# Performance work log

Hardware: AMD Instinct MI355X
Metric: run time of the kernel (lower is better)

## Reference

```python
import jax, jax.numpy as jnp
import numpy as np

B, S, D, H = 2, 2048, 1024, 16
DK = D // H

def setup_inputs() -> dict:
    key = jax.random.key(0)
    ks = jax.random.split(key, 11)
    scale = 0.02
    inp = {
        "Q": jax.random.normal(ks[0], (B, S, D), jnp.float32),
        "K": jax.random.normal(ks[1], (B, S, D), jnp.float32),
        "V": jax.random.normal(ks[2], (B, S, D), jnp.float32),
        "mask": jnp.ones((B, S), jnp.int32),
        "Wq": jax.random.normal(ks[3], (D, D), jnp.float32) * scale,
        "bq": jnp.zeros((D,), jnp.float32),
        "Wk": jax.random.normal(ks[4], (D, D), jnp.float32) * scale,
        "bk": jnp.zeros((D,), jnp.float32),
        "Wv": jax.random.normal(ks[5], (D, D), jnp.float32) * scale,
        "bv": jnp.zeros((D,), jnp.float32),
        "Wo": jax.random.normal(ks[6], (D, D), jnp.float32) * scale,
        "bo": jnp.zeros((D,), jnp.float32),
    }
    return inp

def _split_heads(x):
    # [B,S,D] -> [B,H,S,DK]
    return x.reshape(B, S, H, DK).transpose(0, 2, 1, 3)

def reference(Q, K, V, mask, Wq, bq, Wk, bk, Wv, bv, Wo, bo):
    q = _split_heads(Q @ Wq.T + bq)
    k = _split_heads(K @ Wk.T + bk)
    v = _split_heads(V @ Wv.T + bv)
    scores = jnp.einsum("bhqd,bhkd->bhqk", q, k) / jnp.sqrt(jnp.float32(DK))
    # 2D padding mask -> [B,1,1,S], mask==0 positions set to -inf
    m = mask[:, None, None, :]
    scores = jnp.where(m == 0, -jnp.inf, scores)
    attn_weights = jax.nn.softmax(scores, axis=-1)  # [B,H,S,S]
    attn_output = jnp.einsum("bhqk,bhkd->bhqd", attn_weights, v)
    attn_output = attn_output.transpose(0, 2, 1, 3).reshape(B, S, D)
    output = attn_output @ Wo.T + bo
    return (output, attn_weights)
```

## Files before the change

kernel.cpp:

```cpp
#include <hip/hip_runtime.h>
#include <stdint.h>

#define DEVINL __device__ __forceinline__

typedef float  f32x4  __attribute__((ext_vector_type(4)));
typedef float  f32x16 __attribute__((ext_vector_type(16)));
typedef short  s16x8  __attribute__((ext_vector_type(8)));
typedef unsigned short u16x4 __attribute__((ext_vector_type(4)));
typedef unsigned short u16x8 __attribute__((ext_vector_type(8)));

static constexpr int S = 2048, D = 1024, H = 16;
static constexpr size_t OUT0 = (size_t)2 * S * D;

DEVINL unsigned short f2bf(float f) {
  union { float f; unsigned u; } v; v.f = f;
  unsigned r = v.u + 0x7FFFu + ((v.u >> 16) & 1u);
  return (unsigned short)(r >> 16);
}

DEVINL unsigned cvt_pk_bf16(float lo, float hi) {
  unsigned r;
  asm("v_cvt_pk_bf16_f32 %0, %1, %2" : "=v"(r) : "v"(lo), "v"(hi));
  return r;
}

DEVINL void perm32swap(unsigned& a, unsigned& b) {
#if __has_builtin(__builtin_amdgcn_permlane32_swap)
  auto r = __builtin_amdgcn_permlane32_swap(a, b, false, false);
  a = r[0]; b = r[1];
#else
  asm volatile("v_permlane32_swap_b32 %0, %1" : "+v"(a), "+v"(b));
#endif
}

DEVINL void gload_lds16(const void* g, void* l) {
  __builtin_amdgcn_global_load_lds(
      (const __attribute__((address_space(1))) unsigned int*)g,
      (__attribute__((address_space(3))) unsigned int*)l, 16, 0, 0);
}

DEVINL void cvt_body(const float* __restrict__ src, unsigned short* __restrict__ dst, int i) {
  const f32x4* s4 = (const f32x4*)src;
  f32x4 a = s4[i * 2], b = s4[i * 2 + 1];
  u16x8 o;
  o[0] = f2bf(a[0]); o[1] = f2bf(a[1]); o[2] = f2bf(a[2]); o[3] = f2bf(a[3]);
  o[4] = f2bf(b[0]); o[5] = f2bf(b[1]); o[6] = f2bf(b[2]); o[7] = f2bf(b[3]);
  ((u16x8*)dst)[i] = o;
}

__global__ __launch_bounds__(256) void k_cvt_all(
    const float* __restrict__ Q, const float* __restrict__ K, const float* __restrict__ V,
    const float* __restrict__ Wq, const float* __restrict__ Wk,
    const float* __restrict__ Wv, const float* __restrict__ Wo,
    unsigned short* __restrict__ Xq, unsigned short* __restrict__ Xk,
    unsigned short* __restrict__ Xv,
    unsigned short* __restrict__ WQ, unsigned short* __restrict__ WK,
    unsigned short* __restrict__ WV, unsigned short* __restrict__ WO) {
  int i = blockIdx.x;
  const float* src; unsigned short* dst; int item;
  if (i < 6144) {
    int z = i >> 11;
    item = (i & 2047) * 256 + threadIdx.x;
    src = z == 0 ? Q : z == 1 ? K : V;
    dst = z == 0 ? Xq : z == 1 ? Xk : Xv;
  } else {
    int j = i - 6144, z = j >> 9;
    item = (j & 511) * 256 + threadIdx.x;
    src = z == 0 ? Wq : z == 1 ? Wk : z == 2 ? Wv : Wo;
    dst = z == 0 ? WQ : z == 1 ? WK : z == 2 ? WV : WO;
  }
  cvt_body(src, dst, item);
}

template <int MODE>
DEVINL void gemm_tile(const unsigned short* __restrict__ A,
                      const unsigned short* __restrict__ Bw,
                      const float* __restrict__ bias, void* __restrict__ Cout,
                      int tileM, int tileN, float scl,
                      unsigned short* As, unsigned short* Bs) {
  const int tid = threadIdx.x;
  const int lane = tid & 63, wave = tid >> 6;
  const int wr = wave >> 1, wc = wave & 1;
  const int l15 = lane & 15, l16 = lane >> 4;
  f32x4 acc[4][4] = {};
  for (int k0 = 0; k0 < 1024; k0 += 64) {
#pragma unroll
    for (int p = 0; p < 4; ++p) {
      int c = tid + p * 256;
      int row = c >> 3, cc = (c & 7) ^ (row & 7);
      gload_lds16(A + (((size_t)(tileM + row)) << 10) + k0 + cc * 8, &As[c * 8]);
      gload_lds16(Bw + (((size_t)(tileN + row)) << 10) + k0 + cc * 8, &Bs[c * 8]);
    }
    __syncthreads();
#pragma unroll
    for (int kk = 0; kk < 2; ++kk) {
      s16x8 af[4], bf[4];
#pragma unroll
      for (int i = 0; i < 4; ++i) {
        int r = wr * 64 + i * 16 + l15;
        af[i] = *(const s16x8*)((const char*)As + r * 128 +
                                ((kk * 64 + l16 * 16) ^ ((r & 7) << 4)));
      }
#pragma unroll
      for (int j = 0; j < 4; ++j) {
        int r = wc * 64 + j * 16 + l15;
        bf[j] = *(const s16x8*)((const char*)Bs + r * 128 +
                                ((kk * 64 + l16 * 16) ^ ((r & 7) << 4)));
      }
#pragma unroll
      for (int i = 0; i < 4; ++i)
#pragma unroll
        for (int j = 0; j < 4; ++j)
          acc[i][j] = __builtin_amdgcn_mfma_f32_16x16x32_bf16(af[i], bf[j], acc[i][j], 0, 0, 0);
    }
    __syncthreads();
  }
#pragma unroll
  for (int i = 0; i < 4; ++i) {
#pragma unroll
    for (int j = 0; j < 4; ++j) {
      int n = tileN + wc * 64 + j * 16 + l15;
      float bv = bias[n];
      if (MODE == 2) {
        int m0 = tileM + wr * 64 + i * 16 + l16 * 4;
        int b_ = m0 >> 11, s_ = m0 & 2047;
        int h_ = n >> 6, d_ = n & 63;
        u16x4 o;
#pragma unroll
        for (int r = 0; r < 4; ++r) o[r] = f2bf(acc[i][j][r] + bv);
        *(u16x4*)&((unsigned short*)Cout)[(size_t)(b_ * H + h_) * S * 64 +
                                          (s_ >> 6) * 4096 + d_ * 64 + (s_ & 63)] = o;
      } else {
#pragma unroll
        for (int r = 0; r < 4; ++r) {
          int m = tileM + wr * 64 + i * 16 + l16 * 4 + r;
          float v = (acc[i][j][r] + bv) * scl;
          if (MODE == 0) {
            int b_ = m >> 11, s_ = m & 2047, h_ = n >> 6, d_ = n & 63;
            ((unsigned short*)Cout)[(((size_t)(b_ * H + h_) * S) + s_) * 64 + d_] = f2bf(v);
          } else {
            ((float*)Cout)[(size_t)m * 1024 + n] = v;
          }
        }
      }
    }
  }
}

__global__ __launch_bounds__(256) void k_gemm_qkv(
    const unsigned short* __restrict__ Xq, const unsigned short* __restrict__ Xk,
    const unsigned short* __restrict__ Xv,
    const unsigned short* __restrict__ Wq, const unsigned short* __restrict__ Wk,
    const unsigned short* __restrict__ Wv,
    const float* __restrict__ bq, const float* __restrict__ bk, const float* __restrict__ bv,
    unsigned short* __restrict__ oq, unsigned short* __restrict__ ok,
    unsigned short* __restrict__ vt2) {
  __shared__ alignas(16) unsigned short As[128 * 64];
  __shared__ alignas(16) unsigned short Bs[128 * 64];
  int flat = (blockIdx.z * 32 + blockIdx.y) * 8 + blockIdx.x;
  int swz = (flat & 7) * 96 + (flat >> 3);
  int z = swz >> 8;
  int rem = swz & 255;
  int ty = rem >> 3, tx = rem & 7;
  if (z == 2) {
    gemm_tile<2>(Xv, Wv, bv, vt2, ty * 128, tx * 128, 1.0f, As, Bs);
  } else {
    const unsigned short* A = z == 0 ? Xq : Xk;
    const unsigned short* W = z == 0 ? Wq : Wk;
    const float* bias = z == 0 ? bq : bk;
    unsigned short* o = z == 0 ? oq : ok;
    gemm_tile<0>(A, W, bias, o, ty * 128, tx * 128, z == 0 ? 0.125f : 1.0f, As, Bs);
  }
}

__global__ __launch_bounds__(256) void k_gemm_out(const unsigned short* __restrict__ A,
                                                  const unsigned short* __restrict__ W,
                                                  const float* __restrict__ bias,
                                                  float* __restrict__ Cout) {
  __shared__ alignas(16) unsigned short As[128 * 64];
  __shared__ alignas(16) unsigned short Bs[128 * 64];
  int flat = blockIdx.y * 8 + blockIdx.x;
  int swz = (flat & 7) * 32 + (flat >> 3);
  int ty = swz >> 3, tx = swz & 7;
  gemm_tile<1>(A, W, bias, Cout, ty * 128, tx * 128, 1.0f, As, Bs);
}

__global__ __launch_bounds__(256) void k_attn_fused(const unsigned short* __restrict__ qw,
                                                    const unsigned short* __restrict__ kw,
                                                    const unsigned short* __restrict__ vt2,
                                                    const int* __restrict__ mask,
                                                    unsigned short* __restrict__ aout,
                                                    float* __restrict__ attw) {
  __shared__ alignas(16) char lds[33536];
  unsigned short* Ks = (unsigned short*)lds;
  unsigned short* Vs = (unsigned short*)(lds + 16384);
  float* lsumW = (float*)(lds + 32768);
  float* lsumT = (float*)(lds + 33280);
  float* nl2lW = (float*)(lds + 33408);
  const float LOG2E = 1.44269504f;

  int flat = blockIdx.y * 64 + blockIdx.x;
  int swzb = (flat & 7) * 256 + (flat >> 3);
  const int bh = swzb >> 6, b = bh >> 4, h = bh & 15;
  const int q0 = (swzb & 63) * 32;
  const int tid = threadIdx.x;
  const int lane = tid & 63, w = tid >> 6;
  const int l31 = lane & 31, hi = lane >> 5;

  const unsigned short* kw_bh = kw + (size_t)bh * S * 64;
  const unsigned short* vt_bh = vt2 + (size_t)bh * S * 64;
  const int* mrow = mask + b * S;

  s16x8 qf[4];
  const unsigned short* qbase = qw + ((size_t)bh * S + q0 + l31) * 64 + hi * 8;
#pragma unroll
  for (int kc = 0; kc < 4; ++kc) qf[kc] = *(const s16x8*)(qbase + kc * 16);

  f32x16 oT0 = {}, oT1 = {};
  float lsum = 0.f;
  const int swv = (l31 & 15) << 4;

  for (int t = 0; t < 16; ++t) {
#pragma unroll
    for (int p = 0; p < 4; ++p) {
      int c = tid + p * 256, row = c >> 3, cc = (c & 7) ^ (row & 7);
      gload_lds16(kw_bh + ((size_t)(t * 128 + row)) * 64 + cc * 8, Ks + c * 8);
    }
#pragma unroll
    for (int p = 0; p < 4; ++p) {
      int c = tid + p * 256, row = c >> 4, c16 = (c & 15) ^ (row & 15);
      gload_lds16(vt_bh + (size_t)(t * 2 + (c16 >> 3)) * 4096 + row * 64 + (c16 & 7) * 8,
                  Vs + c * 8);
    }
    __syncthreads();

    const int krow = w * 32 + l31;
    f32x16 sT = {};
#pragma unroll
    for (int kc = 0; kc < 4; ++kc) {
      s16x8 ka = *(const s16x8*)((const char*)Ks + krow * 128 +
                                 ((kc * 32 + hi * 16) ^ ((krow & 7) << 4)));
      sT = __builtin_amdgcn_mfma_f32_32x32x16_bf16(ka, qf[kc], sT, 0, 0, 0);
    }

    int base = t * 128 + w * 32 + 4 * hi;
    int m[16];
    *(int4*)&m[0]  = *(const int4*)&mrow[base];
    *(int4*)&m[4]  = *(const int4*)&mrow[base + 8];
    *(int4*)&m[8]  = *(const int4*)&mrow[base + 16];
    *(int4*)&m[12] = *(const int4*)&mrow[base + 24];

    float e[16];
#pragma unroll
    for (int r = 0; r < 16; ++r) {
      e[r] = m[r] ? exp2f(sT[r] * LOG2E) : 0.f;
      lsum += e[r];
    }

    unsigned x0 = cvt_pk_bf16(e[0], e[1]),   x1 = cvt_pk_bf16(e[2], e[3]);
    unsigned x2 = cvt_pk_bf16(e[4], e[5]),   x3 = cvt_pk_bf16(e[6], e[7]);
    unsigned x4 = cvt_pk_bf16(e[8], e[9]),   x5 = cvt_pk_bf16(e[10], e[11]);
    unsigned x6 = cvt_pk_bf16(e[12], e[13]), x7 = cvt_pk_bf16(e[14], e[15]);
    perm32swap(x0, x2); perm32swap(x1, x3);
    perm32swap(x4, x6); perm32swap(x5, x7);
    union { unsigned u[4]; s16x8 v; } p0u, p1u;
    p0u.u[0] = x0; p0u.u[1] = x1; p0u.u[2] = x2; p0u.u[3] = x3;
    p1u.u[0] = x4; p1u.u[1] = x5; p1u.u[2] = x6; p1u.u[3] = x7;

    const int ko0 = w * 64 + hi * 16, ko1 = w * 64 + 32 + hi * 16;
    const char* Vr0 = (const char*)Vs + l31 * 256;
    const char* Vr1 = (const char*)Vs + (32 + l31) * 256;
    s16x8 va;
    va = *(const s16x8*)(Vr0 + (ko0 ^ swv));
    oT0 = __builtin_amdgcn_mfma_f32_32x32x16_bf16(va, p0u.v, oT0, 0, 0, 0);
    va = *(const s16x8*)(Vr0 + (ko1 ^ swv));
    oT0 = __builtin_amdgcn_mfma_f32_32x32x16_bf16(va, p1u.v, oT0, 0, 0, 0);
    va = *(const s16x8*)(Vr1 + (ko0 ^ swv));
    oT1 = __builtin_amdgcn_mfma_f32_32x32x16_bf16(va, p0u.v, oT1, 0, 0, 0);
    va = *(const s16x8*)(Vr1 + (ko1 ^ swv));
    oT1 = __builtin_amdgcn_mfma_f32_32x32x16_bf16(va, p1u.v, oT1, 0, 0, 0);

    __syncthreads();
  }

  lsum += __shfl_xor(lsum, 32);
  if (hi == 0) lsumW[w * 32 + l31] = lsum;

  {
    char* orow = (char*)lds + w * 8192 + l31 * 256;
#pragma unroll
    for (int rg = 0; rg < 4; ++rg) {
      f32x4 c0, c1;
#pragma unroll
      for (int j = 0; j < 4; ++j) { c0[j] = oT0[rg * 4 + j]; c1[j] = oT1[rg * 4 + j]; }
      *(f32x4*)(orow + ((rg * 32 + hi * 16) ^ swv)) = c0;
      *(f32x4*)(orow + ((128 + rg * 32 + hi * 16) ^ swv)) = c1;
    }
  }
  __syncthreads();

  if (tid < 32) {
    float tot = lsumW[tid] + lsumW[32 + tid] + lsumW[64 + tid] + lsumW[96 + tid];
    lsumT[tid] = tot;
    nl2lW[tid] = __log2f(tot);
  }
  __syncthreads();

  {
    int q = tid >> 3, dg = tid & 7;
    float inv = 1.f / lsumT[q];
    int sq = (q & 15) << 4;
    float s[8] = {};
#pragma unroll
    for (int w4 = 0; w4 < 4; ++w4) {
      const char* prow = (const char*)lds + w4 * 8192 + q * 256;
      f32x4 a = *(const f32x4*)(prow + ((dg * 32) ^ sq));
      f32x4 bb = *(const f32x4*)(prow + ((dg * 32 + 16) ^ sq));
#pragma unroll
      for (int j = 0; j < 4; ++j) { s[j] += a[j]; s[4 + j] += bb[j]; }
    }
    u16x8 ob;
#pragma unroll
    for (int j = 0; j < 8; ++j) ob[j] = f2bf(s[j] * inv);
    *(u16x8*)&aout[((size_t)b * S + q0 + q) * D + h * 64 + dg * 8] = ob;
  }

  float nl2l[16];
#pragma unroll
  for (int r = 0; r < 16; ++r) nl2l[r] = nl2lW[(r & 3) + 8 * (r >> 2) + 4 * hi];

  for (int it = 0; it < 16; ++it) {
    int key0 = it * 128 + w * 32;
    const unsigned short* kbase = kw_bh + (size_t)(key0 + l31) * 64 + hi * 8;
    s16x8 kb[4];
#pragma unroll
    for (int kc = 0; kc < 4; ++kc) kb[kc] = *(const s16x8*)(kbase + kc * 16);
    f32x16 dacc = {};
#pragma unroll
    for (int kc = 0; kc < 4; ++kc)
      dacc = __builtin_amdgcn_mfma_f32_32x32x16_bf16(qf[kc], kb[kc], dacc, 0, 0, 0);

    int key = key0 + l31;
    int mk = mrow[key];
    float* obase = attw + ((size_t)bh * S + q0) * S + key;
#pragma unroll
    for (int r = 0; r < 16; ++r) {
      int row = (r & 3) + 8 * (r >> 2) + 4 * hi;
      float wv = mk ? exp2f(dacc[r] * LOG2E - nl2l[r]) : 0.f;
      __builtin_nontemporal_store(wv, obase + (size_t)row * S);
    }
  }
}

extern "C" void kernel_launch(void* const* d_in, const int* in_sizes, int n_in,
                              void* d_out, int out_size, void* d_ws, size_t ws_size,
                              hipStream_t stream) {
  (void)in_sizes; (void)n_in; (void)out_size; (void)ws_size;
  const float* Q  = (const float*)d_in[0];
  const float* K  = (const float*)d_in[1];
  const float* V  = (const float*)d_in[2];
  const int* mask = (const int*)d_in[3];
  const float* Wq = (const float*)d_in[4];
  const float* bq = (const float*)d_in[5];
  const float* Wk = (const float*)d_in[6];
  const float* bk = (const float*)d_in[7];
  const float* Wv = (const float*)d_in[8];
  const float* bv = (const float*)d_in[9];
  const float* Wo = (const float*)d_in[10];
  const float* bo = (const float*)d_in[11];

  char* ws = (char*)d_ws;
  unsigned short* Xbf  = (unsigned short*)(ws + 0);
  unsigned short* Wbf  = (unsigned short*)(ws + 25165824);
  unsigned short* qws  = (unsigned short*)(ws + 33554432);
  unsigned short* kws  = (unsigned short*)(ws + 41943040);
  unsigned short* vt2  = (unsigned short*)(ws + 50331648);
  unsigned short* aoutb= (unsigned short*)(ws + 8388608);
  float* out0 = (float*)d_out;
  float* attw = (float*)d_out + OUT0;

  k_cvt_all<<<dim3(8192), dim3(256), 0, stream>>>(
      Q, K, V, Wq, Wk, Wv, Wo,
      Xbf, Xbf + 4194304, Xbf + 8388608,
      Wbf, Wbf + 1048576, Wbf + 2097152, Wbf + 3145728);

  k_gemm_qkv<<<dim3(8, 32, 3), dim3(256), 0, stream>>>(
      Xbf, Xbf + 4194304, Xbf + 8388608,
      Wbf, Wbf + 1048576, Wbf + 2097152,
      bq, bk, bv, qws, kws, vt2);

  k_attn_fused<<<dim3(64, 32), dim3(256), 0, stream>>>(qws, kws, vt2, mask, aoutb, attw);

  k_gemm_out<<<dim3(8, 32), dim3(256), 0, stream>>>(aoutb, Wbf + 3145728, bo, out0);
}
```

Baseline: 250.5 us.

## Halve GEMM K-step, drop LDS swizzle, stage V-transpose epilogue through LDS

The shared GEMM tile now steps K by 32 instead of 64, with a plain unswizzled LDS layout and half the LDS footprint for the out-projection kernel. The V projection epilogue writes the bias-added bf16 tile into swizzled LDS and then emits 16-byte coalesced stores in the transposed per-head layout, replacing scattered 8-byte stores. The smaller K step doubles barrier count per tile and the unswizzled 64-byte row stride may cause LDS bank conflicts on fragment reads, while smaller LDS use could raise occupancy.

Measured after the change: 241.7 us. 3.5% less time.

```diff
diff --git a/kernel.cpp b/kernel.cpp
--- a/kernel.cpp
+++ b/kernel.cpp
@@ -76,61 +76,74 @@
 DEVINL void gemm_tile(const unsigned short* __restrict__ A,
                       const unsigned short* __restrict__ Bw,
                       const float* __restrict__ bias, void* __restrict__ Cout,
-                      int tileM, int tileN, float scl,
-                      unsigned short* As, unsigned short* Bs) {
+                      int tileM, int tileN, float scl, char* smem) {
+  unsigned short* As = (unsigned short*)smem;
+  unsigned short* Bs = (unsigned short*)(smem + 8192);
   const int tid = threadIdx.x;
   const int lane = tid & 63, wave = tid >> 6;
   const int wr = wave >> 1, wc = wave & 1;
   const int l15 = lane & 15, l16 = lane >> 4;
   f32x4 acc[4][4] = {};
-  for (int k0 = 0; k0 < 1024; k0 += 64) {
-#pragma unroll
-    for (int p = 0; p < 4; ++p) {
+  for (int k0 = 0; k0 < 1024; k0 += 32) {
+#pragma unroll
+    for (int p = 0; p < 2; ++p) {
       int c = tid + p * 256;
-      int row = c >> 3, cc = (c & 7) ^ (row & 7);
-      gload_lds16(A + (((size_t)(tileM + row)) << 10) + k0 + cc * 8, &As[c * 8]);
-      gload_lds16(Bw + (((size_t)(tileN + row)) << 10) + k0 + cc * 8, &Bs[c * 8]);
+      int row = c >> 2, col = (c & 3) * 8;
+      gload_lds16(A + (((size_t)(tileM + row)) << 10) + k0 + col, &As[c * 8]);
+      gload_lds16(Bw + (((size_t)(tileN + row)) << 10) + k0 + col, &Bs[c * 8]);
     }
     __syncthreads();
-#pragma unroll
-    for (int kk = 0; kk < 2; ++kk) {
-      s16x8 af[4], bf[4];
-#pragma unroll
-      for (int i = 0; i < 4; ++i) {
-        int r = wr * 64 + i * 16 + l15;
-        af[i] = *(const s16x8*)((const char*)As + r * 128 +
-                                ((kk * 64 + l16 * 16) ^ ((r & 7) << 4)));
+    s16x8 af[4], bf[4];
+#pragma unroll
+    for (int i = 0; i < 4; ++i)
+      af[i] = *(const s16x8*)&As[(wr * 64 + i * 16 + l15) * 32 + l16 * 8];
+#pragma unroll
+    for (int i = 0; i < 4; ++i)
+      bf[i] = *(const s16x8*)&Bs[(wc * 64 + i * 16 + l15) * 32 + l16 * 8];
+#pragma unroll
+    for (int i = 0; i < 4; ++i)
+#pragma unroll
+      for (int j = 0; j < 4; ++j)
+        acc[i][j] = __builtin_amdgcn_mfma_f32_16x16x32_bf16(af[i], bf[j], acc[i][j], 0, 0, 0);
+    __syncthreads();
+  }
+
+  if (MODE == 2) {
+    unsigned short* T = (unsigned short*)smem;
+#pragma unroll
+    for (int i = 0; i < 4; ++i)
+#pragma unroll
+      for (int j = 0; j < 4; ++j) {
+        int n = wc * 64 + j * 16 + l15;
+        float bv = bias[tileN + n];
+        int m0 = wr * 64 + i * 16 + l16 * 4;
+        u16x4 o;
+#pragma unroll
+        for (int r = 0; r < 4; ++r) o[r] = f2bf(acc[i][j][r] + bv);
+        *(u16x4*)((char*)T + n * 256 + ((m0 * 2) ^ ((n & 15) << 4))) = o;
       }
+    __syncthreads();
+    {
+      int n = tid >> 1, mh = tid & 1;
+      int d = (tileN + n) & 63, h_ = (tileN + n) >> 6;
+      int b_ = tileM >> 11;
+      int kt_ = (((tileM & 2047) + mh * 64) >> 6);
+      unsigned short* dst = (unsigned short*)Cout + (size_t)(b_ * H + h_) * S * 64 +
+                            (size_t)kt_ * 4096 + d * 64;
+#pragma unroll
+      for (int k = 0; k < 8; ++k) {
+        int mc = mh * 64 + k * 8;
+        u16x8 v = *(const u16x8*)((const char*)T + n * 256 + ((mc * 2) ^ ((n & 15) << 4)));
+        *(u16x8*)(dst + k * 8) = v;
+      }
+    }
+  } else {
+#pragma unroll
+    for (int i = 0; i < 4; ++i) {
 #pragma unroll
       for (int j = 0; j < 4; ++j) {
-        int r = wc * 64 + j * 16 + l15;
-        bf[j] = *(const s16x8*)((const char*)Bs + r * 128 +
-                                ((kk * 64 + l16 * 16) ^ ((r & 7) << 4)));
-      }
-#pragma unroll
-      for (int i = 0; i < 4; ++i)
-#pragma unroll
-        for (int j = 0; j < 4; ++j)
-          acc[i][j] = __builtin_amdgcn_mfma_f32_16x16x32_bf16(af[i], bf[j], acc[i][j], 0, 0, 0);
-    }
-    __syncthreads();
-  }
-#pragma unroll
-  for (int i = 0; i < 4; ++i) {
-#pragma unroll
-    for (int j = 0; j < 4; ++j) {
-      int n = tileN + wc * 64 + j * 16 + l15;
-      float bv = bias[n];
-      if (MODE == 2) {
-        int m0 = tileM + wr * 64 + i * 16 + l16 * 4;
-        int b_ = m0 >> 11, s_ = m0 & 2047;
-        int h_ = n >> 6, d_ = n & 63;
-        u16x4 o;
-#pragma unroll
-        for (int r = 0; r < 4; ++r) o[r] = f2bf(acc[i][j][r] + bv);
-        *(u16x4*)&((unsigned short*)Cout)[(size_t)(b_ * H + h_) * S * 64 +
-                                          (s_ >> 6) * 4096 + d_ * 64 + (s_ & 63)] = o;
-      } else {
+        int n = tileN + wc * 64 + j * 16 + l15;
+        float bv = bias[n];
 #pragma unroll
         for (int r = 0; r < 4; ++r) {
           int m = tileM + wr * 64 + i * 16 + l16 * 4 + r;
@@ -155,21 +168,20 @@
     const float* __restrict__ bq, const float* __restrict__ bk, const float* __restrict__ bv,
     unsigned short* __restrict__ oq, unsigned short* __restrict__ ok,
     unsigned short* __restrict__ vt2) {
-  __shared__ alignas(16) unsigned short As[128 * 64];
-  __shared__ alignas(16) unsigned short Bs[128 * 64];
+  __shared__ alignas(16) char smem[32768];
   int flat = (blockIdx.z * 32 + blockIdx.y) * 8 + blockIdx.x;
   int swz = (flat & 7) * 96 + (flat >> 3);
   int z = swz >> 8;
   int rem = swz & 255;
   int ty = rem >> 3, tx = rem & 7;
   if (z == 2) {
-    gemm_tile<2>(Xv, Wv, bv, vt2, ty * 128, tx * 128, 1.0f, As, Bs);
+    gemm_tile<2>(Xv, Wv, bv, vt2, ty * 128, tx * 128, 1.0f, smem);
   } else {
     const unsigned short* A = z == 0 ? Xq : Xk;
     const unsigned short* W = z == 0 ? Wq : Wk;
     const float* bias = z == 0 ? bq : bk;
     unsigned short* o = z == 0 ? oq : ok;
-    gemm_tile<0>(A, W, bias, o, ty * 128, tx * 128, z == 0 ? 0.125f : 1.0f, As, Bs);
+    gemm_tile<0>(A, W, bias, o, ty * 128, tx * 128, z == 0 ? 0.125f : 1.0f, smem);
   }
 }
 
@@ -177,12 +189,11 @@
                                                   const unsigned short* __restrict__ W,
                                                   const float* __restrict__ bias,
                                                   float* __restrict__ Cout) {
-  __shared__ alignas(16) unsigned short As[128 * 64];
-  __shared__ alignas(16) unsigned short Bs[128 * 64];
+  __shared__ alignas(16) char smem[16384];
   int flat = blockIdx.y * 8 + blockIdx.x;
   int swz = (flat & 7) * 32 + (flat >> 3);
   int ty = swz >> 3, tx = swz & 7;
-  gemm_tile<1>(A, W, bias, Cout, ty * 128, tx * 128, 1.0f, As, Bs);
+  gemm_tile<1>(A, W, bias, Cout, ty * 128, tx * 128, 1.0f, smem);
 }
 
 __global__ __launch_bounds__(256) void k_attn_fused(const unsigned short* __restrict__ qw,
```
